# Optimization experiments

Measured on AMD Instinct MI355X. Metric: run time of the kernel, lower is better.

Reference implementation:

```python
import jax, jax.numpy as jnp
import numpy as np

B, D_IN, D_OUT = 131072, 256, 256

def setup_inputs() -> dict:
    key = jax.random.key(0)
    k1, k2, k3 = jax.random.split(key, 3)
    x = jax.random.normal(k1, (B, D_IN), dtype=jnp.float32)
    # One weight row / bias scalar per SingleNeuron, concatenated: [D_OUT, D_IN], [D_OUT]
    bound = 1.0 / np.sqrt(D_IN)  # nn.Linear default init scale
    W = jax.random.uniform(k2, (D_OUT, D_IN), dtype=jnp.float32, minval=-bound, maxval=bound)
    b = jax.random.uniform(k3, (D_OUT,), dtype=jnp.float32, minval=-bound, maxval=bound)
    return {"x": x, "W": W, "b": b}

def reference(x, W, b):
    # Fused equivalent of looping per-neuron Linear(in,1), stack(dim=1), squeeze, relu
    return jax.nn.relu(jnp.einsum('bi,oi->bo', x, W) + b)
```

## Files before the change

### kernel.cpp

```cpp
#include <hip/hip_runtime.h>


typedef __attribute__((ext_vector_type(16))) float f32x16;
typedef __attribute__((ext_vector_type(8))) __bf16 bf16x8;

#define MFMA(a, b, c) \
    (c) = __builtin_amdgcn_mfma_f32_32x32x16_bf16((a), (b), (c), 0, 0, 0)

__device__ __forceinline__ void cvt8(const float4& A, const float4& B,
                                     bf16x8& hi, bf16x8& lo) {
    const float f[8] = {A.x, A.y, A.z, A.w, B.x, B.y, B.z, B.w};
#pragma unroll
    for (int j = 0; j < 8; ++j) {
        const unsigned int u = __builtin_bit_cast(unsigned int, f[j]);
        hi[j] = __builtin_bit_cast(__bf16, (unsigned short)(u >> 16));
        const float hf = __builtin_bit_cast(float, u & 0xffff0000u);
        const float lf = f[j] - hf;
        lo[j] = __builtin_bit_cast(__bf16,
                    (unsigned short)(__builtin_bit_cast(unsigned int, lf) >> 16));
    }
}

__device__ __forceinline__ void gload16(const float* g, float* l) {
    __builtin_amdgcn_global_load_lds(
        (const __attribute__((address_space(1))) void*)g,
        (__attribute__((address_space(3))) void*)l, 16, 0, 0);
}

__global__ __launch_bounds__(256)
void wprep_kernel(const float* __restrict__ W,
                  __bf16* __restrict__ whi, __bf16* __restrict__ wlo) {
    const int wv = (int)blockIdx.x * 4 + (threadIdx.x >> 6);
    const int l  = threadIdx.x & 63;
    const int t  = wv & 15;
    const int j  = (wv >> 4) & 1;
    const int wn = (wv >> 5) & 1;
    const int ct = wv >> 6;
    const int n  = ct * 128 + wn * 64 + j * 32 + (l & 31);
    const int k  = t * 16 + (l >> 5) * 8;
    const float4 A = *(const float4*)(W + n * 256 + k);
    const float4 B = *(const float4*)(W + n * 256 + k + 4);
    bf16x8 hi, lo;
    cvt8(A, B, hi, lo);
    *(bf16x8*)(whi + wv * 512 + l * 8) = hi;
    *(bf16x8*)(wlo + wv * 512 + l * 8) = lo;
}

__global__ __launch_bounds__(256)
void gemm_mfma_kernel(const float* __restrict__ x,
                      const __bf16* __restrict__ whi,
                      const __bf16* __restrict__ wlo,
                      const float* __restrict__ bias,
                      float* __restrict__ out) {
    __shared__ float xs[2][4096];

    const int tid  = threadIdx.x;
    const int lane = tid & 63;
    const int wid  = tid >> 6;
    const int wm   = wid >> 1;
    const int wn   = wid & 1;

    const int bid = (int)blockIdx.x;
    const int swz = (bid & 7) * 256 + (bid >> 3);
    const int rt  = swz >> 1;
    const int ct  = swz & 1;

    const int r31 = lane & 31;
    const int g   = lane >> 5;
    const long row0 = (long)rt * 128;

    const int Gbase = wid * 64 + lane;
    const int m0 = wm * 64 + r31;
    const int m1 = m0 + 32;
    const int sw = r31 & 7;

    f32x16 acc[2][2];
#pragma unroll
    for (int i = 0; i < 2; ++i)
#pragma unroll
        for (int j = 0; j < 2; ++j)
#pragma unroll
            for (int r = 0; r < 16; ++r) acc[i][j][r] = 0.f;

    const int fbase0 = (ct * 4 + wn * 2) * 16;
    const __bf16* whip = whi + (long)lane * 8;
    const __bf16* wlop = wlo + (long)lane * 8;

    auto STAGE = [&](int b, int chunk) {
#pragma unroll
        for (int j = 0; j < 4; ++j) {
            const int G = j * 256 + Gbase;
            const int m = G >> 3;
            const int cs = (G & 7) ^ (m & 7);
            const float* gp = x + (row0 + m) * 256 + chunk * 32 + cs * 4;
            float* lp = &xs[b][(j * 256 + wid * 64) * 4];
            gload16(gp, lp);
        }
    };

    auto COMPUTE = [&](int b, int chunk) {
#pragma unroll
        for (int t = 0; t < 2; ++t) {
            const int ks = chunk * 2 + t;
            const int c0 = t * 4 + g * 2;
            const float* xb = &xs[b][0];
            const float4 A0a = *(const float4*)(xb + m0 * 32 + ((c0 ^ sw) * 4));
            const float4 A0b = *(const float4*)(xb + m0 * 32 + (((c0 + 1) ^ sw) * 4));
            const float4 A1a = *(const float4*)(xb + m1 * 32 + ((c0 ^ sw) * 4));
            const float4 A1b = *(const float4*)(xb + m1 * 32 + (((c0 + 1) ^ sw) * 4));
            bf16x8 ah0, al0, ah1, al1;
            cvt8(A0a, A0b, ah0, al0);
            cvt8(A1a, A1b, ah1, al1);

            const long f0 = (long)(fbase0 + ks) * 512;
            const long f1 = f0 + 16 * 512;
            const bf16x8 bh0 = *(const bf16x8*)(whip + f0);
            const bf16x8 bl0 = *(const bf16x8*)(wlop + f0);
            const bf16x8 bh1 = *(const bf16x8*)(whip + f1);
            const bf16x8 bl1 = *(const bf16x8*)(wlop + f1);

            MFMA(ah0, bh0, acc[0][0]); MFMA(ah0, bh1, acc[0][1]);
            MFMA(ah1, bh0, acc[1][0]); MFMA(ah1, bh1, acc[1][1]);
            MFMA(ah0, bl0, acc[0][0]); MFMA(ah0, bl1, acc[0][1]);
            MFMA(ah1, bl0, acc[1][0]); MFMA(ah1, bl1, acc[1][1]);
            MFMA(al0, bh0, acc[0][0]); MFMA(al0, bh1, acc[0][1]);
            MFMA(al1, bh0, acc[1][0]); MFMA(al1, bh1, acc[1][1]);
        }
    };

    STAGE(0, 0);
    asm volatile("s_waitcnt vmcnt(0)" ::: "memory");
    __syncthreads();
    for (int c = 0; c < 7; ++c) {
        STAGE((c + 1) & 1, c + 1);
        COMPUTE(c & 1, c);
        asm volatile("s_waitcnt vmcnt(0)" ::: "memory");
        __syncthreads();
    }
    COMPUTE(1, 7);

    const int  ocol0 = ct * 128 + wn * 64;
    const long orow0 = (long)rt * 128 + wm * 64;
    const float bj0 = bias[ocol0 + r31];
    const float bj1 = bias[ocol0 + 32 + r31];

#pragma unroll
    for (int i = 0; i < 2; ++i) {
#pragma unroll
        for (int r = 0; r < 16; ++r) {
            const int rowf = (r & 3) + 8 * (r >> 2) + 4 * g;
            const long row = orow0 + i * 32 + rowf;
            float v0 = acc[i][0][r] + bj0;
            float v1 = acc[i][1][r] + bj1;
            v0 = v0 > 0.f ? v0 : 0.f;
            v1 = v1 > 0.f ? v1 : 0.f;
            out[row * 256 + ocol0 + r31]      = v0;
            out[row * 256 + ocol0 + 32 + r31] = v1;
        }
    }
}

extern "C" void kernel_launch(void* const* d_in, const int* in_sizes, int n_in,
                              void* d_out, int out_size, void* d_ws, size_t ws_size,
                              hipStream_t stream) {
    (void)n_in; (void)ws_size; (void)out_size;
    const float* x = (const float*)d_in[0];
    const float* W = (const float*)d_in[1];
    const float* b = (const float*)d_in[2];
    float* out = (float*)d_out;

    __bf16* whi = (__bf16*)d_ws;
    __bf16* wlo = whi + 65536;

    wprep_kernel<<<32, 256, 0, stream>>>(W, whi, wlo);

    const int M = in_sizes[0] / 256;
    const int grid = (M / 128) * 2;
    gemm_mfma_kernel<<<grid, 256, 0, stream>>>(x, whi, wlo, b, out);
}
```

Before: 262.0 us.

## Triple-buffer x tiles with partial vmcnt waits and early weight loads

Moves from double to triple buffering of the x tile in LDS, prefetching two chunks ahead with a partial vmcnt wait so that only the oldest async load must finish before each chunk. Weight fragments for both k-steps of a chunk are issued from global memory before the next stage is launched, and the loop is fully unrolled. The intent is to overlap more x loading with the MFMA work and to hide global weight-load latency. In exchange it uses 50% more LDS, which may lower occupancy, and the vmcnt counts depend on how the weight loads and staging loads are ordered.

Result: faster. 256.0 us (-2.3%).

```diff
diff --git a/kernel.cpp b/kernel.cpp
--- a/kernel.cpp
+++ b/kernel.cpp
@@ -52,7 +52,7 @@
                       const __bf16* __restrict__ wlo,
                       const float* __restrict__ bias,
                       float* __restrict__ out) {
-    __shared__ float xs[2][4096];
+    __shared__ float xs[3][4096];
 
     const int tid  = threadIdx.x;
     const int lane = tid & 63;
@@ -98,46 +98,59 @@
         }
     };
 
-    auto COMPUTE = [&](int b, int chunk) {
-#pragma unroll
-        for (int t = 0; t < 2; ++t) {
-            const int ks = chunk * 2 + t;
-            const int c0 = t * 4 + g * 2;
-            const float* xb = &xs[b][0];
-            const float4 A0a = *(const float4*)(xb + m0 * 32 + ((c0 ^ sw) * 4));
-            const float4 A0b = *(const float4*)(xb + m0 * 32 + (((c0 + 1) ^ sw) * 4));
-            const float4 A1a = *(const float4*)(xb + m1 * 32 + ((c0 ^ sw) * 4));
-            const float4 A1b = *(const float4*)(xb + m1 * 32 + (((c0 + 1) ^ sw) * 4));
-            bf16x8 ah0, al0, ah1, al1;
-            cvt8(A0a, A0b, ah0, al0);
-            cvt8(A1a, A1b, ah1, al1);
-
-            const long f0 = (long)(fbase0 + ks) * 512;
-            const long f1 = f0 + 16 * 512;
-            const bf16x8 bh0 = *(const bf16x8*)(whip + f0);
-            const bf16x8 bl0 = *(const bf16x8*)(wlop + f0);
-            const bf16x8 bh1 = *(const bf16x8*)(whip + f1);
-            const bf16x8 bl1 = *(const bf16x8*)(wlop + f1);
-
-            MFMA(ah0, bh0, acc[0][0]); MFMA(ah0, bh1, acc[0][1]);
-            MFMA(ah1, bh0, acc[1][0]); MFMA(ah1, bh1, acc[1][1]);
-            MFMA(ah0, bl0, acc[0][0]); MFMA(ah0, bl1, acc[0][1]);
-            MFMA(ah1, bl0, acc[1][0]); MFMA(ah1, bl1, acc[1][1]);
-            MFMA(al0, bh0, acc[0][0]); MFMA(al0, bh1, acc[0][1]);
-            MFMA(al1, bh0, acc[1][0]); MFMA(al1, bh1, acc[1][1]);
-        }
+    auto TSTEP = [&](const float* xb, int t,
+                     const bf16x8& bh0, const bf16x8& bl0,
+                     const bf16x8& bh1, const bf16x8& bl1) {
+        const int c0 = t * 4 + g * 2;
+        const float4 A0a = *(const float4*)(xb + m0 * 32 + ((c0 ^ sw) * 4));
+        const float4 A0b = *(const float4*)(xb + m0 * 32 + (((c0 + 1) ^ sw) * 4));
+        const float4 A1a = *(const float4*)(xb + m1 * 32 + ((c0 ^ sw) * 4));
+        const float4 A1b = *(const float4*)(xb + m1 * 32 + (((c0 + 1) ^ sw) * 4));
+        bf16x8 ah0, al0, ah1, al1;
+        cvt8(A0a, A0b, ah0, al0);
+        cvt8(A1a, A1b, ah1, al1);
+        MFMA(ah0, bh0, acc[0][0]); MFMA(ah0, bh1, acc[0][1]);
+        MFMA(ah1, bh0, acc[1][0]); MFMA(ah1, bh1, acc[1][1]);
+        MFMA(ah0, bl0, acc[0][0]); MFMA(ah0, bl1, acc[0][1]);
+        MFMA(ah1, bl0, acc[1][0]); MFMA(ah1, bl1, acc[1][1]);
+        MFMA(al0, bh0, acc[0][0]); MFMA(al0, bh1, acc[0][1]);
+        MFMA(al1, bh0, acc[1][0]); MFMA(al1, bh1, acc[1][1]);
     };
 
+#define CHUNK(c, VM)                                                          \
+    {                                                                         \
+        asm volatile("s_waitcnt vmcnt(" VM ")" ::: "memory");                 \
+        __builtin_amdgcn_s_barrier();                                         \
+        const long f0 = (long)(fbase0 + (c) * 2) * 512;                       \
+        const long f1 = f0 + 16 * 512;                                        \
+        const long h0 = (long)(fbase0 + (c) * 2 + 1) * 512;                   \
+        const long h1 = h0 + 16 * 512;                                        \
+        const bf16x8 B0h0 = *(const bf16x8*)(whip + f0);                      \
+        const bf16x8 B0l0 = *(const bf16x8*)(wlop + f0);                      \
+        const bf16x8 B0h1 = *(const bf16x8*)(whip + f1);                      \
+        const bf16x8 B0l1 = *(const bf16x8*)(wlop + f1);                      \
+        const bf16x8 B1h0 = *(const bf16x8*)(whip + h0);                      \
+        const bf16x8 B1l0 = *(const bf16x8*)(wlop + h0);                      \
+        const bf16x8 B1h1 = *(const bf16x8*)(whip + h1);                      \
+        const bf16x8 B1l1 = *(const bf16x8*)(wlop + h1);                      \
+        __builtin_amdgcn_sched_barrier(0);                                    \
+        if ((c) + 2 < 8) STAGE(((c) + 2) % 3, (c) + 2);                       \
+        const float* xb = &xs[(c) % 3][0];                                    \
+        TSTEP(xb, 0, B0h0, B0l0, B0h1, B0l1);                                 \
+        TSTEP(xb, 1, B1h0, B1l0, B1h1, B1l1);                                 \
+    }
+
     STAGE(0, 0);
-    asm volatile("s_waitcnt vmcnt(0)" ::: "memory");
-    __syncthreads();
-    for (int c = 0; c < 7; ++c) {
-        STAGE((c + 1) & 1, c + 1);
-        COMPUTE(c & 1, c);
-        asm volatile("s_waitcnt vmcnt(0)" ::: "memory");
-        __syncthreads();
-    }
-    COMPUTE(1, 7);
+    STAGE(1, 1);
+    CHUNK(0, "4")
+    CHUNK(1, "4")
+    CHUNK(2, "4")
+    CHUNK(3, "4")
+    CHUNK(4, "4")
+    CHUNK(5, "4")
+    CHUNK(6, "4")
+    CHUNK(7, "0")
+#undef CHUNK
 
     const int  ocol0 = ct * 128 + wn * 64;
     const long orow0 = (long)rt * 128 + wm * 64;
```
